# Optimization experiments

Measured on AMD Instinct MI355X. Metric: run time of the kernel, lower is better.

Reference implementation:

```python
import jax, jax.numpy as jnp
import numpy as np

N_HEADS = 8
TANH_CLIP = 10.0


def setup_inputs() -> dict:
    key = jax.random.key(0)
    ks = jax.random.split(key, 7)
    B, N, D = 128, 1000, 512
    embeddings = jax.random.normal(ks[0], (B, N, D), dtype=jnp.float32)
    step_context = jax.random.normal(ks[1], (B, 1, 2 * D), dtype=jnp.float32)
    # action mask: True = feasible action; guarantee at least one feasible per row
    action_mask = jax.random.uniform(ks[2], (B, 1, N)) > 0.3
    action_mask = action_mask.at[:, :, 0].set(True)
    s = 0.02
    W_node = jax.random.normal(ks[3], (D, 3 * D), dtype=jnp.float32) * s
    W_fixed = jax.random.normal(ks[4], (D, D), dtype=jnp.float32) * s
    W_step = jax.random.normal(ks[5], (2 * D, D), dtype=jnp.float32) * s
    W_out = jax.random.normal(ks[6], (D, D), dtype=jnp.float32) * s
    return {"embeddings": embeddings, "step_context": step_context,
            "action_mask": action_mask, "W_node": W_node, "W_fixed": W_fixed,
            "W_step": W_step, "W_out": W_out}


def reference(embeddings, step_context, action_mask, W_node, W_fixed, W_step, W_out):
    B, N, D = embeddings.shape
    H = N_HEADS
    hd = D // H
    neg_inf = jnp.float32(-jnp.inf)

    # --- precompute (Decoder._precompute) ---
    graph_embed = embeddings.mean(axis=1)                      # [B, D]
    kvl = embeddings @ W_node                                  # [B, N, 3D]
    _gk, gv, logit_key = jnp.split(kvl, 3, axis=-1)
    # source bug: glimpse_key variable is overwritten with glimpse_val, and
    # attention is called with key = value = glimpse_val
    KV = gv.reshape(B, N, H, hd).transpose(0, 2, 1, 3)         # [B, H, N, hd]
    graph_context = (graph_embed @ W_fixed)[:, None, :]        # [B, 1, D]

    # --- per-step query (Decoder._get_log_p) ---
    query = graph_context + step_context @ W_step              # [B, 1, D]
    q = query.reshape(B, 1, H, hd).transpose(0, 2, 1, 3)       # [B, H, 1, hd]

    # --- inner MHA (scaled_dot_product_attention with boolean mask) ---
    scores = jnp.einsum('bhqs,bhns->bhqn', q, KV) / jnp.sqrt(jnp.float32(hd))
    scores = jnp.where(action_mask[:, None, :, :], scores, neg_inf)  # [B,H,1,N]
    attn = jax.nn.softmax(scores, axis=-1)
    heads = jnp.einsum('bhqn,bhns->bhqs', attn, KV)            # [B, H, 1, hd]
    heads = heads.transpose(0, 2, 1, 3).reshape(B, 1, D)       # [B, 1, D]

    # --- glimpse projection and logit head ---
    glimpse = heads @ W_out                                    # [B, 1, D]
    logits = jnp.einsum('bqd,bnd->bqn', glimpse, logit_key) / jnp.sqrt(jnp.float32(D))
    logits = jnp.tanh(logits) * TANH_CLIP
    logits = jnp.where(action_mask, logits, neg_inf)
    return jax.nn.log_softmax(logits, axis=-1)                 # [B, 1, N]
```

## Files before the change

### kernel.cpp

```cpp
#include <hip/hip_runtime.h>
#include <math.h>

#define B 128
#define N 1000
#define D 512
#define H 8
#define NCH 10
#define CHK 100
#define NCHM 25
#define CHKM 40

#define OFF_QW    0
#define OFF_PMEAN (OFF_QW + B*H*D)
#define OFF_PAE   (OFF_PMEAN + B*NCHM*D)
#define OFF_P     (OFF_PAE + B*NCH*H*D)
#define OFF_ZC    (OFF_P + B*N*H)
#define OFF_GW    (OFF_ZC + B*NCH*H)
#define OFF_LG    (OFF_GW + B*D)
#define OFF_LMAX  (OFF_LG + B*N)
#define OFF_LSUM  (OFF_LMAX + B*NCH)

__device__ inline float dot4(float4 a, float4 b){
    float r = a.x * b.x;
    r = fmaf(a.y, b.y, r);
    r = fmaf(a.z, b.z, r);
    r = fmaf(a.w, b.w, r);
    return r;
}

__global__ void k1_partial_mean(const float* __restrict__ emb, float* __restrict__ ws){
    int chunk = blockIdx.x, b = blockIdx.y, t = threadIdx.x;
    const float4* e4 = (const float4*)emb + ((size_t)b * N + (size_t)chunk * CHKM) * (D / 4) + t;
    float4 a0 = make_float4(0,0,0,0), a1 = a0, a2 = a0, a3 = a0;
    for (int n = 0; n < CHKM; n += 4) {
        float4 v0 = e4[(size_t)(n + 0) * (D / 4)];
        float4 v1 = e4[(size_t)(n + 1) * (D / 4)];
        float4 v2 = e4[(size_t)(n + 2) * (D / 4)];
        float4 v3 = e4[(size_t)(n + 3) * (D / 4)];
        a0.x += v0.x; a0.y += v0.y; a0.z += v0.z; a0.w += v0.w;
        a1.x += v1.x; a1.y += v1.y; a1.z += v1.z; a1.w += v1.w;
        a2.x += v2.x; a2.y += v2.y; a2.z += v2.z; a2.w += v2.w;
        a3.x += v3.x; a3.y += v3.y; a3.z += v3.z; a3.w += v3.w;
    }
    float4 acc;
    acc.x = (a0.x + a1.x) + (a2.x + a3.x);
    acc.y = (a0.y + a1.y) + (a2.y + a3.y);
    acc.z = (a0.z + a1.z) + (a2.z + a3.z);
    acc.w = (a0.w + a1.w) + (a2.w + a3.w);
    ((float4*)(ws + OFF_PMEAN + (size_t)(b * NCHM + chunk) * D))[t] = acc;
}

__global__ void k2_prep(const float* __restrict__ stepc, const float* __restrict__ Wnode,
                        const float* __restrict__ Wfix, const float* __restrict__ Wstep,
                        float* __restrict__ ws){
    int b = blockIdx.x, d = threadIdx.x;
    __shared__ float ge[D];
    __shared__ float q[D];
    float s = 0.f;
    #pragma unroll
    for (int c = 0; c < NCHM; ++c) s += ws[OFF_PMEAN + (size_t)(b * NCHM + c) * D + d];
    ge[d] = s * (1.0f / N);
    __syncthreads();
    float a0 = 0.f, a1 = 0.f, a2 = 0.f, a3 = 0.f;
    for (int k = 0; k < D; k += 4) {
        a0 = fmaf(ge[k],     Wfix[(size_t)k * D + d],       a0);
        a1 = fmaf(ge[k + 1], Wfix[(size_t)(k + 1) * D + d], a1);
        a2 = fmaf(ge[k + 2], Wfix[(size_t)(k + 2) * D + d], a2);
        a3 = fmaf(ge[k + 3], Wfix[(size_t)(k + 3) * D + d], a3);
    }
    const float* sc = stepc + (size_t)b * 2 * D;
    for (int k = 0; k < 2 * D; k += 4) {
        a0 = fmaf(sc[k],     Wstep[(size_t)k * D + d],       a0);
        a1 = fmaf(sc[k + 1], Wstep[(size_t)(k + 1) * D + d], a1);
        a2 = fmaf(sc[k + 2], Wstep[(size_t)(k + 2) * D + d], a2);
        a3 = fmaf(sc[k + 3], Wstep[(size_t)(k + 3) * D + d], a3);
    }
    q[d] = (a0 + a1) + (a2 + a3);
    __syncthreads();
    const float* wrow = Wnode + (size_t)d * 3 * D + D;
    #pragma unroll
    for (int h = 0; h < H; ++h) {
        float a = 0.f;
        const float* qh = q + h * 64;
        const float* wh = wrow + h * 64;
        #pragma unroll 8
        for (int s2 = 0; s2 < 64; ++s2) a = fmaf(qh[s2], wh[s2], a);
        ws[OFF_QW + ((size_t)b * H + h) * D + d] = a;
    }
}

__global__ __launch_bounds__(256) void kb_scores(const float* __restrict__ emb,
        const unsigned char* __restrict__ mask, float* __restrict__ ws){
    const int cg = blockIdx.x, b = blockIdx.y, t = threadIdx.x;
    const int w = t >> 6, l = t & 63, g = l >> 4;
    __shared__ float part[CHK][4][H];
    __shared__ float zsh[H];
    if (t < H) zsh[t] = 0.f;
    float4 qlo[H], qhi[H];
    {
        const float* qb = ws + OFF_QW + (size_t)b * H * D;
        #pragma unroll
        for (int h = 0; h < H; ++h) {
            qlo[h] = *(const float4*)(qb + (size_t)h * D + 4 * l);
            qhi[h] = *(const float4*)(qb + (size_t)h * D + 256 + 4 * l);
        }
    }
    const float* embb = emb + ((size_t)b * N + (size_t)cg * CHK) * D;
    for (int i = 0; i < CHK / 4; ++i) {
        const int nl = 4 * i + w;
        const float4* er = (const float4*)(embb + (size_t)nl * D) + l;
        float4 e0 = er[0];
        float4 e1 = er[64];
        float s[H];
        #pragma unroll
        for (int h = 0; h < H; ++h)
            s[h] = dot4(e0, qlo[h]) + dot4(e1, qhi[h]);
        #pragma unroll
        for (int o = 1; o <= 8; o <<= 1) {
            #pragma unroll
            for (int h = 0; h < H; ++h) s[h] += __shfl_xor(s[h], o);
        }
        if ((l & 15) == 0) {
            *(float4*)&part[nl][g][0] = make_float4(s[0], s[1], s[2], s[3]);
            *(float4*)&part[nl][g][4] = make_float4(s[4], s[5], s[6], s[7]);
        }
    }
    __syncthreads();
    const unsigned char* mb = mask + (size_t)b * N + cg * CHK;
    float* pout = ws + OFF_P + ((size_t)b * N + (size_t)cg * CHK) * H;
    for (int slot = t; slot < CHK * H; slot += 256) {
        int r = slot >> 3, h = slot & 7;
        float v = (part[r][0][h] + part[r][1][h]) + (part[r][2][h] + part[r][3][h]);
        bool m = mb[r] != 0;
        float pe = m ? __expf(v * 0.125f) : 0.f;
        pout[slot] = pe;
        atomicAdd(&zsh[h], pe);
    }
    __syncthreads();
    if (t < H) ws[OFF_ZC + ((size_t)b * NCH + cg) * H + t] = zsh[t];
}

__global__ __launch_bounds__(256) void kb_pv(const float* __restrict__ emb,
        float* __restrict__ ws){
    const int cg = blockIdx.x, b = blockIdx.y, t = threadIdx.x;
    __shared__ float p_lds[CHK][H];
    {
        const float* pin = ws + OFF_P + ((size_t)b * N + (size_t)cg * CHK) * H;
        for (int s = t; s < CHK * H; s += 256) ((float*)p_lds)[s] = pin[s];
    }
    __syncthreads();
    const float* embb = emb + ((size_t)b * N + (size_t)cg * CHK) * D;
    float2 acc[H];
    #pragma unroll
    for (int h = 0; h < H; ++h) acc[h] = make_float2(0.f, 0.f);
    const float2* ecol = (const float2*)embb + t;
    #pragma unroll 2
    for (int i = 0; i < CHK; ++i) {
        float2 e = ecol[(size_t)i * (D / 2)];
        float4 pa = *(const float4*)&p_lds[i][0];
        float4 pb = *(const float4*)&p_lds[i][4];
        acc[0].x = fmaf(pa.x, e.x, acc[0].x); acc[0].y = fmaf(pa.x, e.y, acc[0].y);
        acc[1].x = fmaf(pa.y, e.x, acc[1].x); acc[1].y = fmaf(pa.y, e.y, acc[1].y);
        acc[2].x = fmaf(pa.z, e.x, acc[2].x); acc[2].y = fmaf(pa.z, e.y, acc[2].y);
        acc[3].x = fmaf(pa.w, e.x, acc[3].x); acc[3].y = fmaf(pa.w, e.y, acc[3].y);
        acc[4].x = fmaf(pb.x, e.x, acc[4].x); acc[4].y = fmaf(pb.x, e.y, acc[4].y);
        acc[5].x = fmaf(pb.y, e.x, acc[5].x); acc[5].y = fmaf(pb.y, e.y, acc[5].y);
        acc[6].x = fmaf(pb.z, e.x, acc[6].x); acc[6].y = fmaf(pb.z, e.y, acc[6].y);
        acc[7].x = fmaf(pb.w, e.x, acc[7].x); acc[7].y = fmaf(pb.w, e.y, acc[7].y);
    }
    float2* paeb = (float2*)(ws + OFF_PAE) + ((size_t)(b * NCH + cg) * H) * (D / 2) + t;
    #pragma unroll
    for (int h = 0; h < H; ++h) paeb[(size_t)h * (D / 2)] = acc[h];
}

__global__ __launch_bounds__(512) void kd_post(const float* __restrict__ Wnode,
        const float* __restrict__ Wout, float* __restrict__ ws){
    int b = blockIdx.x, t = threadIdx.x;
    __shared__ float ae[H * D];
    __shared__ float heads[D];
    __shared__ float gl[D];
    __shared__ float iZ[H];
    if (t < H) {
        float Z = 0.f;
        #pragma unroll
        for (int c = 0; c < NCH; ++c)
            Z += ws[OFF_ZC + ((size_t)b * NCH + c) * H + t];
        iZ[t] = 1.0f / Z;
    }
    __syncthreads();
    #pragma unroll
    for (int h = 0; h < H; ++h) {
        float s = 0.f;
        #pragma unroll
        for (int c = 0; c < NCH; ++c)
            s += ws[OFF_PAE + (((size_t)b * NCH + c) * H + h) * (size_t)D + t];
        ae[h * D + t] = s * iZ[h];
    }
    __syncthreads();
    {
        int h = t >> 6;
        const float* aeh = ae + h * D;
        const float* col = Wnode + 512 + t;
        float a0 = 0.f, a1 = 0.f, a2 = 0.f, a3 = 0.f;
        for (int d = 0; d < D; d += 4) {
            a0 = fmaf(aeh[d],     col[(size_t)d * (3 * D)],       a0);
            a1 = fmaf(aeh[d + 1], col[(size_t)(d + 1) * (3 * D)], a1);
            a2 = fmaf(aeh[d + 2], col[(size_t)(d + 2) * (3 * D)], a2);
            a3 = fmaf(aeh[d + 3], col[(size_t)(d + 3) * (3 * D)], a3);
        }
        heads[t] = (a0 + a1) + (a2 + a3);
    }
    __syncthreads();
    {
        float a0 = 0.f, a1 = 0.f, a2 = 0.f, a3 = 0.f;
        for (int d = 0; d < D; d += 4) {
            a0 = fmaf(heads[d],     Wout[(size_t)d * D + t],       a0);
            a1 = fmaf(heads[d + 1], Wout[(size_t)(d + 1) * D + t], a1);
            a2 = fmaf(heads[d + 2], Wout[(size_t)(d + 2) * D + t], a2);
            a3 = fmaf(heads[d + 3], Wout[(size_t)(d + 3) * D + t], a3);
        }
        gl[t] = (a0 + a1) + (a2 + a3);
    }
    __syncthreads();
    {
        const float* wrow = Wnode + (size_t)t * (3 * D) + 2 * D;
        float a0 = 0.f, a1 = 0.f, a2 = 0.f, a3 = 0.f;
        for (int e = 0; e < D; e += 4) {
            a0 = fmaf(gl[e],     wrow[e],     a0);
            a1 = fmaf(gl[e + 1], wrow[e + 1], a1);
            a2 = fmaf(gl[e + 2], wrow[e + 2], a2);
            a3 = fmaf(gl[e + 3], wrow[e + 3], a3);
        }
        ws[OFF_GW + (size_t)b * D + t] = (a0 + a1) + (a2 + a3);
    }
}

__global__ __launch_bounds__(256) void kc_logits(const float* __restrict__ emb,
        const unsigned char* __restrict__ mask, float* __restrict__ ws){
    const int cg = blockIdx.x, b = blockIdx.y, t = threadIdx.x;
    const int w = t >> 6, l = t & 63;
    __shared__ float wm[4], wsum[4];
    float4 glo, ghi;
    {
        const float* gb = ws + OFF_GW + (size_t)b * D;
        glo = *(const float4*)(gb + 4 * l);
        ghi = *(const float4*)(gb + 256 + 4 * l);
    }
    const float* embb = emb + ((size_t)b * N + (size_t)cg * CHK) * D;
    const unsigned char* mb = mask + (size_t)b * N + cg * CHK;
    float m = -INFINITY, s = 0.f;
    for (int i = 0; i < CHK / 4; ++i) {
        const int nl = 4 * i + w;
        const float4* er = (const float4*)(embb + (size_t)nl * D) + l;
        float4 e0 = er[0];
        float4 e1 = er[64];
        float a = dot4(e0, glo) + dot4(e1, ghi);
        #pragma unroll
        for (int o = 32; o > 0; o >>= 1) a += __shfl_xor(a, o);
        bool mk = mb[nl] != 0;
        float lg = mk ? tanhf(a * 0.044194173824159216f) * 10.0f : -INFINITY;
        if (l == 0) ws[OFF_LG + (size_t)b * N + cg * CHK + nl] = lg;
        if (mk) {
            float mn = fmaxf(m, lg);
            s = s * __expf(m - mn) + __expf(lg - mn);
            m = mn;
        }
    }
    if (l == 0) { wm[w] = m; wsum[w] = s; }
    __syncthreads();
    if (t == 0) {
        float M = -INFINITY;
        #pragma unroll
        for (int i = 0; i < 4; ++i) M = fmaxf(M, wm[i]);
        float S = 0.f;
        #pragma unroll
        for (int i = 0; i < 4; ++i)
            if (wm[i] != -INFINITY) S += wsum[i] * __expf(wm[i] - M);
        ws[OFF_LMAX + (size_t)b * NCH + cg] = M;
        ws[OFF_LSUM + (size_t)b * NCH + cg] = S;
    }
}

__global__ void k8_out(const float* __restrict__ ws, float* __restrict__ out){
    int b = blockIdx.x, t = threadIdx.x;
    __shared__ float Ls;
    if (t == 0) {
        float M = -INFINITY;
        #pragma unroll
        for (int c = 0; c < NCH; ++c)
            M = fmaxf(M, ws[OFF_LMAX + (size_t)b * NCH + c]);
        float S = 0.f;
        #pragma unroll
        for (int c = 0; c < NCH; ++c) {
            float m = ws[OFF_LMAX + (size_t)b * NCH + c];
            if (m != -INFINITY) S += __expf(m - M) * ws[OFF_LSUM + (size_t)b * NCH + c];
        }
        Ls = M + __logf(S);
    }
    __syncthreads();
    float L = Ls;
    for (int j = t; j < N; j += 256)
        out[(size_t)b * N + j] = fmaxf(ws[OFF_LG + (size_t)b * N + j] - L, -1e30f);
}

extern "C" void kernel_launch(void* const* d_in, const int* in_sizes, int n_in,
                              void* d_out, int out_size, void* d_ws, size_t ws_size,
                              hipStream_t stream) {
    const float* emb   = (const float*)d_in[0];
    const float* stepc = (const float*)d_in[1];
    const unsigned char* mask = (const unsigned char*)d_in[2];
    const float* Wnode = (const float*)d_in[3];
    const float* Wfix  = (const float*)d_in[4];
    const float* Wstep = (const float*)d_in[5];
    const float* Wout  = (const float*)d_in[6];
    float* out = (float*)d_out;
    float* ws  = (float*)d_ws;

    k1_partial_mean<<<dim3(NCHM, B), 128, 0, stream>>>(emb, ws);
    k2_prep<<<dim3(B), 512, 0, stream>>>(stepc, Wnode, Wfix, Wstep, ws);
    kb_scores<<<dim3(NCH, B), 256, 0, stream>>>(emb, mask, ws);
    kb_pv<<<dim3(NCH, B), 256, 0, stream>>>(emb, ws);
    kd_post<<<dim3(B), 512, 0, stream>>>(Wnode, Wout, ws);
    kc_logits<<<dim3(NCH, B), 256, 0, stream>>>(emb, mask, ws);
    k8_out<<<dim3(B), 256, 0, stream>>>(ws, out);
}
```

Baseline: 366.8 us.

## Convert embeddings to bf16 once and fuse scores with PV pass

The mean kernel now also writes a bf16 copy of the embeddings into workspace. The attention and logit kernels read that half-size copy instead of the fp32 input. The score and PV kernels are merged so the softmax weights stay in shared memory instead of round-tripping through global memory. This cuts repeated reads of the large embedding tensor but adds a full bf16 write pass and lowers the precision of the dot products.

```diff
diff --git a/kernel.cpp b/kernel.cpp
--- a/kernel.cpp
+++ b/kernel.cpp
@@ -7,46 +7,49 @@
 #define H 8
 #define NCH 10
 #define CHK 100
-#define NCHM 25
-#define CHKM 40
-
-#define OFF_QW    0
+#define NCHM 20
+#define CHKM 50
+
+#define EMB16_FLOATS (B*N*D/2)
+#define OFF_QW    EMB16_FLOATS
 #define OFF_PMEAN (OFF_QW + B*H*D)
 #define OFF_PAE   (OFF_PMEAN + B*NCHM*D)
-#define OFF_P     (OFF_PAE + B*NCH*H*D)
-#define OFF_ZC    (OFF_P + B*N*H)
+#define OFF_ZC    (OFF_PAE + B*NCH*H*D)
 #define OFF_GW    (OFF_ZC + B*NCH*H)
 #define OFF_LG    (OFF_GW + B*D)
 #define OFF_LMAX  (OFF_LG + B*N)
 #define OFF_LSUM  (OFF_LMAX + B*NCH)
 
-__device__ inline float dot4(float4 a, float4 b){
-    float r = a.x * b.x;
-    r = fmaf(a.y, b.y, r);
-    r = fmaf(a.z, b.z, r);
-    r = fmaf(a.w, b.w, r);
-    return r;
-}
-
-__global__ void k1_partial_mean(const float* __restrict__ emb, float* __restrict__ ws){
+__device__ inline unsigned short f2bf(float f){
+    unsigned int u = __float_as_uint(f);
+    u = (u + 0x7FFFu + ((u >> 16) & 1u)) >> 16;
+    return (unsigned short)u;
+}
+__device__ inline float bflo(unsigned int u){ return __uint_as_float(u << 16); }
+__device__ inline float bfhi(unsigned int u){ return __uint_as_float(u & 0xffff0000u); }
+
+__global__ void k1_convert_mean(const float* __restrict__ emb, float* __restrict__ ws){
     int chunk = blockIdx.x, b = blockIdx.y, t = threadIdx.x;
-    const float4* e4 = (const float4*)emb + ((size_t)b * N + (size_t)chunk * CHKM) * (D / 4) + t;
-    float4 a0 = make_float4(0,0,0,0), a1 = a0, a2 = a0, a3 = a0;
-    for (int n = 0; n < CHKM; n += 4) {
-        float4 v0 = e4[(size_t)(n + 0) * (D / 4)];
+    const size_t row0 = (size_t)b * N + (size_t)chunk * CHKM;
+    const float4* e4 = (const float4*)emb + row0 * (D / 4) + t;
+    ushort2* o2 = (ushort2*)ws;
+    float4 a0 = make_float4(0,0,0,0), a1 = a0;
+    for (int n = 0; n < CHKM; n += 2) {
+        float4 v0 = e4[(size_t)n * (D / 4)];
         float4 v1 = e4[(size_t)(n + 1) * (D / 4)];
-        float4 v2 = e4[(size_t)(n + 2) * (D / 4)];
-        float4 v3 = e4[(size_t)(n + 3) * (D / 4)];
         a0.x += v0.x; a0.y += v0.y; a0.z += v0.z; a0.w += v0.w;
         a1.x += v1.x; a1.y += v1.y; a1.z += v1.z; a1.w += v1.w;
-        a2.x += v2.x; a2.y += v2.y; a2.z += v2.z; a2.w += v2.w;
-        a3.x += v3.x; a3.y += v3.y; a3.z += v3.z; a3.w += v3.w;
+        size_t w0 = (row0 + n) * (D / 4) + t;
+        ushort2 lo0 = { f2bf(v0.x), f2bf(v0.y) }, hi0 = { f2bf(v0.z), f2bf(v0.w) };
+        ushort2 lo1 = { f2bf(v1.x), f2bf(v1.y) }, hi1 = { f2bf(v1.z), f2bf(v1.w) };
+        o2[w0 * 2]     = lo0;
+        o2[w0 * 2 + 1] = hi0;
+        o2[(w0 + (D / 4)) * 2]     = lo1;
+        o2[(w0 + (D / 4)) * 2 + 1] = hi1;
     }
     float4 acc;
-    acc.x = (a0.x + a1.x) + (a2.x + a3.x);
-    acc.y = (a0.y + a1.y) + (a2.y + a3.y);
-    acc.z = (a0.z + a1.z) + (a2.z + a3.z);
-    acc.w = (a0.w + a1.w) + (a2.w + a3.w);
+    acc.x = a0.x + a1.x; acc.y = a0.y + a1.y;
+    acc.z = a0.z + a1.z; acc.w = a0.w + a1.w;
     ((float4*)(ws + OFF_PMEAN + (size_t)(b * NCHM + chunk) * D))[t] = acc;
 }
 
@@ -89,88 +92,83 @@
     }
 }
 
-__global__ __launch_bounds__(256) void kb_scores(const float* __restrict__ emb,
-        const unsigned char* __restrict__ mask, float* __restrict__ ws){
+__global__ __launch_bounds__(256) void kb_attn(const unsigned char* __restrict__ mask,
+        float* __restrict__ ws){
     const int cg = blockIdx.x, b = blockIdx.y, t = threadIdx.x;
     const int w = t >> 6, l = t & 63, g = l >> 4;
     __shared__ float part[CHK][4][H];
+    __shared__ float p_lds[CHK][H];
     __shared__ float zsh[H];
     if (t < H) zsh[t] = 0.f;
-    float4 qlo[H], qhi[H];
-    {
-        const float* qb = ws + OFF_QW + (size_t)b * H * D;
-        #pragma unroll
-        for (int h = 0; h < H; ++h) {
-            qlo[h] = *(const float4*)(qb + (size_t)h * D + 4 * l);
-            qhi[h] = *(const float4*)(qb + (size_t)h * D + 256 + 4 * l);
-        }
-    }
-    const float* embb = emb + ((size_t)b * N + (size_t)cg * CHK) * D;
+    const float* qb = ws + OFF_QW + (size_t)b * H * D + 8 * l;
+#define QD(h) float4 qa##h = *(const float4*)(qb + (h) * D); \
+              float4 qb##h = *(const float4*)(qb + (h) * D + 4);
+    QD(0) QD(1) QD(2) QD(3) QD(4) QD(5) QD(6) QD(7)
+#undef QD
+    const unsigned int* e16 = (const unsigned int*)ws;
+    const size_t rowu = D / 2;
+    const size_t base = ((size_t)b * N + (size_t)cg * CHK) * rowu;
     for (int i = 0; i < CHK / 4; ++i) {
         const int nl = 4 * i + w;
-        const float4* er = (const float4*)(embb + (size_t)nl * D) + l;
-        float4 e0 = er[0];
-        float4 e1 = er[64];
-        float s[H];
-        #pragma unroll
-        for (int h = 0; h < H; ++h)
-            s[h] = dot4(e0, qlo[h]) + dot4(e1, qhi[h]);
+        const uint4 u = *(const uint4*)(e16 + base + (size_t)nl * rowu + 4 * l);
+        float e0 = bflo(u.x), e1 = bfhi(u.x), e2 = bflo(u.y), e3 = bfhi(u.y);
+        float e4v = bflo(u.z), e5 = bfhi(u.z), e6 = bflo(u.w), e7 = bfhi(u.w);
+        float s0, s1, s2, s3, s4, s5, s6, s7;
+#define DOT(h, dst) { \
+        float r = e0 * qa##h.x; r = fmaf(e1, qa##h.y, r); r = fmaf(e2, qa##h.z, r); \
+        r = fmaf(e3, qa##h.w, r); r = fmaf(e4v, qb##h.x, r); r = fmaf(e5, qb##h.y, r); \
+        r = fmaf(e6, qb##h.z, r); r = fmaf(e7, qb##h.w, r); dst = r; }
+        DOT(0, s0) DOT(1, s1) DOT(2, s2) DOT(3, s3)
+        DOT(4, s4) DOT(5, s5) DOT(6, s6) DOT(7, s7)
+#undef DOT
         #pragma unroll
         for (int o = 1; o <= 8; o <<= 1) {
-            #pragma unroll
-            for (int h = 0; h < H; ++h) s[h] += __shfl_xor(s[h], o);
+            s0 += __shfl_xor(s0, o); s1 += __shfl_xor(s1, o);
+            s2 += __shfl_xor(s2, o); s3 += __shfl_xor(s3, o);
+            s4 += __shfl_xor(s4, o); s5 += __shfl_xor(s5, o);
+            s6 += __shfl_xor(s6, o); s7 += __shfl_xor(s7, o);
         }
         if ((l & 15) == 0) {
-            *(float4*)&part[nl][g][0] = make_float4(s[0], s[1], s[2], s[3]);
-            *(float4*)&part[nl][g][4] = make_float4(s[4], s[5], s[6], s[7]);
+            *(float4*)&part[nl][g][0] = make_float4(s0, s1, s2, s3);
+            *(float4*)&part[nl][g][4] = make_float4(s4, s5, s6, s7);
         }
     }
     __syncthreads();
     const unsigned char* mb = mask + (size_t)b * N + cg * CHK;
-    float* pout = ws + OFF_P + ((size_t)b * N + (size_t)cg * CHK) * H;
     for (int slot = t; slot < CHK * H; slot += 256) {
         int r = slot >> 3, h = slot & 7;
         float v = (part[r][0][h] + part[r][1][h]) + (part[r][2][h] + part[r][3][h]);
         bool m = mb[r] != 0;
         float pe = m ? __expf(v * 0.125f) : 0.f;
-        pout[slot] = pe;
+        p_lds[r][h] = pe;
         atomicAdd(&zsh[h], pe);
     }
     __syncthreads();
     if (t < H) ws[OFF_ZC + ((size_t)b * NCH + cg) * H + t] = zsh[t];
-}
-
-__global__ __launch_bounds__(256) void kb_pv(const float* __restrict__ emb,
-        float* __restrict__ ws){
-    const int cg = blockIdx.x, b = blockIdx.y, t = threadIdx.x;
-    __shared__ float p_lds[CHK][H];
-    {
-        const float* pin = ws + OFF_P + ((size_t)b * N + (size_t)cg * CHK) * H;
-        for (int s = t; s < CHK * H; s += 256) ((float*)p_lds)[s] = pin[s];
-    }
-    __syncthreads();
-    const float* embb = emb + ((size_t)b * N + (size_t)cg * CHK) * D;
-    float2 acc[H];
-    #pragma unroll
-    for (int h = 0; h < H; ++h) acc[h] = make_float2(0.f, 0.f);
-    const float2* ecol = (const float2*)embb + t;
-    #pragma unroll 2
-    for (int i = 0; i < CHK; ++i) {
-        float2 e = ecol[(size_t)i * (D / 2)];
-        float4 pa = *(const float4*)&p_lds[i][0];
-        float4 pb = *(const float4*)&p_lds[i][4];
-        acc[0].x = fmaf(pa.x, e.x, acc[0].x); acc[0].y = fmaf(pa.x, e.y, acc[0].y);
-        acc[1].x = fmaf(pa.y, e.x, acc[1].x); acc[1].y = fmaf(pa.y, e.y, acc[1].y);
-        acc[2].x = fmaf(pa.z, e.x, acc[2].x); acc[2].y = fmaf(pa.z, e.y, acc[2].y);
-        acc[3].x = fmaf(pa.w, e.x, acc[3].x); acc[3].y = fmaf(pa.w, e.y, acc[3].y);
-        acc[4].x = fmaf(pb.x, e.x, acc[4].x); acc[4].y = fmaf(pb.x, e.y, acc[4].y);
-        acc[5].x = fmaf(pb.y, e.x, acc[5].x); acc[5].y = fmaf(pb.y, e.y, acc[5].y);
-        acc[6].x = fmaf(pb.z, e.x, acc[6].x); acc[6].y = fmaf(pb.z, e.y, acc[6].y);
-        acc[7].x = fmaf(pb.w, e.x, acc[7].x); acc[7].y = fmaf(pb.w, e.y, acc[7].y);
-    }
-    float2* paeb = (float2*)(ws + OFF_PAE) + ((size_t)(b * NCH + cg) * H) * (D / 2) + t;
-    #pragma unroll
-    for (int h = 0; h < H; ++h) paeb[(size_t)h * (D / 2)] = acc[h];
+    {
+        float2 acc[H];
+        #pragma unroll
+        for (int h = 0; h < H; ++h) acc[h] = make_float2(0.f, 0.f);
+        const unsigned int* ecol = e16 + base + t;
+        #pragma unroll 2
+        for (int i = 0; i < CHK; ++i) {
+            unsigned int u = ecol[(size_t)i * rowu];
+            float ex = bflo(u), ey = bfhi(u);
+            float4 pa = *(const float4*)&p_lds[i][0];
+            float4 pb = *(const float4*)&p_lds[i][4];
+            acc[0].x = fmaf(pa.x, ex, acc[0].x); acc[0].y = fmaf(pa.x, ey, acc[0].y);
+            acc[1].x = fmaf(pa.y, ex, acc[1].x); acc[1].y = fmaf(pa.y, ey, acc[1].y);
+            acc[2].x = fmaf(pa.z, ex, acc[2].x); acc[2].y = fmaf(pa.z, ey, acc[2].y);
+            acc[3].x = fmaf(pa.w, ex, acc[3].x); acc[3].y = fmaf(pa.w, ey, acc[3].y);
+            acc[4].x = fmaf(pb.x, ex, acc[4].x); acc[4].y = fmaf(pb.x, ey, acc[4].y);
+            acc[5].x = fmaf(pb.y, ex, acc[5].x); acc[5].y = fmaf(pb.y, ey, acc[5].y);
+            acc[6].x = fmaf(pb.z, ex, acc[6].x); acc[6].y = fmaf(pb.z, ey, acc[6].y);
+            acc[7].x = fmaf(pb.w, ex, acc[7].x); acc[7].y = fmaf(pb.w, ey, acc[7].y);
+        }
+        float2* paeb = (float2*)(ws + OFF_PAE) + ((size_t)(b * NCH + cg) * H) * (D / 2) + t;
+        #pragma unroll
+        for (int h = 0; h < H; ++h) paeb[(size_t)h * (D / 2)] = acc[h];
+    }
 }
 
 __global__ __launch_bounds__(512) void kd_post(const float* __restrict__ Wnode,
@@ -235,26 +233,33 @@
     }
 }
 
-__global__ __launch_bounds__(256) void kc_logits(const float* __restrict__ emb,
-        const unsigned char* __restrict__ mask, float* __restrict__ ws){
+__global__ __launch_bounds__(256) void kc_logits(const unsigned char* __restrict__ mask,
+        float* __restrict__ ws){
     const int cg = blockIdx.x, b = blockIdx.y, t = threadIdx.x;
     const int w = t >> 6, l = t & 63;
     __shared__ float wm[4], wsum[4];
-    float4 glo, ghi;
-    {
-        const float* gb = ws + OFF_GW + (size_t)b * D;
-        glo = *(const float4*)(gb + 4 * l);
-        ghi = *(const float4*)(gb + 256 + 4 * l);
-    }
-    const float* embb = emb + ((size_t)b * N + (size_t)cg * CHK) * D;
+    float4 ga, gb;
+    {
+        const float* gp = ws + OFF_GW + (size_t)b * D + 8 * l;
+        ga = *(const float4*)gp;
+        gb = *(const float4*)(gp + 4);
+    }
+    const unsigned int* e16 = (const unsigned int*)ws;
+    const size_t rowu = D / 2;
+    const size_t base = ((size_t)b * N + (size_t)cg * CHK) * rowu;
     const unsigned char* mb = mask + (size_t)b * N + cg * CHK;
     float m = -INFINITY, s = 0.f;
     for (int i = 0; i < CHK / 4; ++i) {
         const int nl = 4 * i + w;
-        const float4* er = (const float4*)(embb + (size_t)nl * D) + l;
-        float4 e0 = er[0];
-        float4 e1 = er[64];
-        float a = dot4(e0, glo) + dot4(e1, ghi);
+        const uint4 u = *(const uint4*)(e16 + base + (size_t)nl * rowu + 4 * l);
+        float a = bflo(u.x) * ga.x;
+        a = fmaf(bfhi(u.x), ga.y, a);
+        a = fmaf(bflo(u.y), ga.z, a);
+        a = fmaf(bfhi(u.y), ga.w, a);
+        a = fmaf(bflo(u.z), gb.x, a);
+        a = fmaf(bfhi(u.z), gb.y, a);
+        a = fmaf(bflo(u.w), gb.z, a);
+        a = fmaf(bfhi(u.w), gb.w, a);
         #pragma unroll
         for (int o = 32; o > 0; o >>= 1) a += __shfl_xor(a, o);
         bool mk = mb[nl] != 0;
@@ -316,11 +321,10 @@
     float* out = (float*)d_out;
     float* ws  = (float*)d_ws;
 
-    k1_partial_mean<<<dim3(NCHM, B), 128, 0, stream>>>(emb, ws);
+    k1_convert_mean<<<dim3(NCHM, B), 128, 0, stream>>>(emb, ws);
     k2_prep<<<dim3(B), 512, 0, stream>>>(stepc, Wnode, Wfix, Wstep, ws);
-    kb_scores<<<dim3(NCH, B), 256, 0, stream>>>(emb, mask, ws);
-    kb_pv<<<dim3(NCH, B), 256, 0, stream>>>(emb, ws);
+    kb_attn<<<dim3(NCH, B), 256, 0, stream>>>(mask, ws);
     kd_post<<<dim3(B), 512, 0, stream>>>(Wnode, Wout, ws);
-    kc_logits<<<dim3(NCH, B), 256, 0, stream>>>(emb, mask, ws);
+    kc_logits<<<dim3(NCH, B), 256, 0, stream>>>(mask, ws);
     k8_out<<<dim3(B), 256, 0, stream>>>(ws, out);
 }
```

After: 353.9 us. 1.04x faster.
